# Kernel optimization log

Hardware: AMD Instinct MI355X
Metric: run time of the kernel (lower is better)

Reference implementation:

```python
import jax, jax.numpy as jnp
import numpy as np
import math

D_MODEL = 768
D_STATE = 16
D_CONV = 4
EXPAND = 2
D_INNER = EXPAND * D_MODEL
DT_RANK = math.ceil(D_MODEL / 16)
B_SZ, SEQ = 2, 2048


def setup_inputs() -> dict:
    key = jax.random.key(0)
    ks = jax.random.split(key, 10)
    s = 0.02
    inp = {
        "input_states": jax.random.normal(ks[0], (B_SZ, SEQ, D_MODEL), jnp.float32),
        "in_proj_w": jax.random.normal(ks[1], (2 * D_INNER, D_MODEL), jnp.float32) * s,
        "conv_w": jax.random.normal(ks[2], (D_INNER, 1, D_CONV), jnp.float32) * s,
        "conv_b": jnp.zeros((D_INNER,), jnp.float32),
        "x_proj_w": jax.random.normal(ks[3], (DT_RANK + 2 * D_STATE, D_INNER), jnp.float32) * s,
        "dt_proj_w": jax.random.normal(ks[4], (D_INNER, DT_RANK), jnp.float32) * s,
        "dt_proj_b": jax.random.normal(ks[5], (D_INNER,), jnp.float32) * 0.1,
        # S4D-real style init: A_log = log(1..d_state) per channel
        "A_log": jnp.log(jnp.broadcast_to(jnp.arange(1, D_STATE + 1, dtype=jnp.float32), (D_INNER, D_STATE))),
        "D": jnp.ones((D_INNER,), jnp.float32),
        "out_proj_w": jax.random.normal(ks[6], (D_MODEL, D_INNER), jnp.float32) * s,
        "context_len": 2,
    }
    return inp


def _silu(x):
    return x * jax.nn.sigmoid(x)


def _chain_tree_scan(w, x):
    # first-order linear recurrence h_t = w_t * h_{t-1} + x_t along last axis
    # (w_0 is ignored by construction of the associative combine)
    def comb(l, r):
        al, bl = l
        ar, br = r
        return (ar * al, ar * bl + br)
    _, h = jax.lax.associative_scan(comb, (w, x), axis=-1)
    return h


def reference(input_states, in_proj_w, conv_w, conv_b, x_proj_w,
              dt_proj_w, dt_proj_b, A_log, D, out_proj_w, context_len):
    # context_len == 2 -> chain-tree branch (identity BFS order, parent[i]=i-1)
    b, L, dm = input_states.shape
    di, n = A_log.shape[0], A_log.shape[1]

    proj = jnp.einsum('bld,ed->ble', input_states, in_proj_w)  # [b,l,2*di]
    proj = jnp.transpose(proj, (0, 2, 1))                      # [b,2*di,l]
    hidden, gate = jnp.split(proj, 2, axis=1)                  # each [b,di,l]

    # causal depthwise conv1d (pad left d_conv-1, truncate to seq_len)
    hidden = jax.lax.conv_general_dilated(
        hidden, conv_w, window_strides=(1,), padding=[(D_CONV - 1, 0)],
        dimension_numbers=('NCH', 'OIH', 'NCH'), feature_group_count=di)
    hidden = _silu(hidden + conv_b[None, :, None])             # [b,di,l]

    ssm = jnp.einsum('bdl,ed->ble', hidden, x_proj_w)          # [b,l,dt_rank+2n]
    dt, Bm, Cm = jnp.split(ssm, [DT_RANK, DT_RANK + n], axis=-1)
    dt = jax.nn.softplus(jnp.einsum('blr,dr->bld', dt, dt_proj_w) + dt_proj_b)
    dt = jnp.transpose(dt, (0, 2, 1))                          # [b,di,l]

    A = -jnp.exp(A_log.astype(jnp.float32))                    # [di,n]
    dA = jnp.exp(A[None, :, None, :] * dt[:, :, :, None])      # [b,di,l,n]
    dBu = dt[:, :, :, None] * Bm[:, None, :, :] * hidden[:, :, :, None]  # [b,di,l,n]

    # rearrange 'b d l n -> b (d n) l'
    w = jnp.transpose(dA, (0, 1, 3, 2)).reshape(b, di * n, L)
    fin = jnp.transpose(dBu, (0, 1, 3, 2)).reshape(b, di * n, L)

    fin_f = jnp.flip(fin, axis=-1)
    w_f = jnp.roll(jnp.flip(w, axis=-1), 1, axis=-1)

    h = _chain_tree_scan(w_f, fin_f)
    # feature_out2 (edge_weight == w_f via identity gather) * 0.3 + feature_out1
    fout = 1.3 * h

    fout = jnp.flip(fout, axis=-1)                              # [b,(d n),l]
    fout = fout.reshape(b, di, n, L)
    fout = jnp.transpose(fout, (0, 3, 1, 2))                    # [b,l,d,n]

    scan_out = jnp.einsum('bldn,bln->bld', fout, Cm)            # [b,l,di]
    scan_out = jnp.transpose(scan_out, (0, 2, 1))               # [b,di,l]

    y = scan_out + hidden * D[None, :, None]
    y = y * _silu(gate)
    out = jnp.einsum('bdl,ed->ble', y, out_proj_w)              # [b,l,d_model]
    return out
```

## Files before the change

kernel.cpp:

```cpp
#include <hip/hip_runtime.h>
#include <hip/hip_bf16.h>

#define DI     1536
#define DM     768
#define E2     3072
#define NST    16
#define LSEQ   2048
#define NB     2
#define NLB    4096
#define SSMW   80
#define DTRANK 48
#define NC     32
#define CP     64

typedef unsigned short u16;
typedef unsigned int   u32;
typedef __attribute__((ext_vector_type(8))) __bf16 bf16x8;
typedef __attribute__((ext_vector_type(4))) float  f32x4;

__device__ __forceinline__ float b2f(u16 u) {
  union { u32 i; float f; } v; v.i = ((u32)u) << 16; return v.f;
}
__device__ __forceinline__ u16 f2b(float f) {
  union { float f; u32 i; } v; v.f = f;
  u32 r = v.i + 0x7FFFu + ((v.i >> 16) & 1u);
  return (u16)(r >> 16);
}
__device__ __forceinline__ void gld16(const u16* g, u16* l) {
  __builtin_amdgcn_global_load_lds(
      (const __attribute__((address_space(1))) void*)g,
      (__attribute__((address_space(3))) void*)l, 16, 0, 0);
}
__device__ __forceinline__ float silu_f(float x) {
  return x / (1.f + __expf(-x));
}

#define B2F_LO(w) __uint_as_float(((u32)(w)) << 16)
#define B2F_HI(w) __uint_as_float(((u32)(w)) & 0xFFFF0000u)

#define ROWSUM16(p)                                                                               \
  asm("v_add_f32 %0, %1, %2 row_ror:8 row_mask:0xf bank_mask:0xf" : "=v"(p) : "v"(p), "v"(p));    \
  asm("v_add_f32 %0, %1, %2 row_ror:4 row_mask:0xf bank_mask:0xf" : "=v"(p) : "v"(p), "v"(p));    \
  asm("v_add_f32 %0, %1, %2 row_ror:2 row_mask:0xf bank_mask:0xf" : "=v"(p) : "v"(p), "v"(p));    \
  asm("v_add_f32 %0, %1, %2 row_ror:1 row_mask:0xf bank_mask:0xf" : "=v"(p) : "v"(p), "v"(p));

__global__ __launch_bounds__(256) void castk(const float* __restrict__ in,
                                             u16* __restrict__ out, int n) {
  int i = (blockIdx.x * 256 + threadIdx.x) * 4;
  if (i >= n) return;
  float4 v = *(const float4*)(in + i);
  u32 lo = (u32)f2b(v.x) | ((u32)f2b(v.y) << 16);
  u32 hi = (u32)f2b(v.z) | ((u32)f2b(v.w) << 16);
  uint2 pk; pk.x = lo; pk.y = hi;
  *(uint2*)(out + i) = pk;
}

__global__ __launch_bounds__(256) void castwdt(const float* __restrict__ in,
                                               const float* __restrict__ bias,
                                               u16* __restrict__ out) {
  int i = blockIdx.x * 256 + threadIdx.x;
  int row = i >> 6, col = i & 63;
  float v = (col < 48) ? in[row * 48 + col] : (col == 48 ? bias[row] : 0.f);
  out[i] = f2b(v);
}

template<int CMODE>
__global__ __launch_bounds__(256) void gemm_bt(const u16* __restrict__ A,
                                               const u16* __restrict__ B,
                                               void* __restrict__ Cp,
                                               int M, int N, int K) {
  __shared__ __align__(16) u16 a_s[128 * 32];
  __shared__ __align__(16) u16 b_s[128 * 32];
  const int tid = threadIdx.x, lane = tid & 63, w = tid >> 6;
  const int m0 = blockIdx.x * 128, n0 = blockIdx.y * 128;
  const int wm = w >> 1, wn = w & 1;
  f32x4 acc[4][4];
#pragma unroll
  for (int i = 0; i < 4; i++)
#pragma unroll
    for (int j = 0; j < 4; j++) acc[i][j] = (f32x4){0.f, 0.f, 0.f, 0.f};

  const int rA = lane >> 2;
  const int c8 = (lane & 3) * 8;
  const int fr = lane & 15;
  const int fk = (lane >> 4) * 8;

  for (int k0 = 0; k0 < K; k0 += 32) {
#pragma unroll
    for (int j = 0; j < 2; j++) {
      int rr = (w * 2 + j) * 16;
      gld16(A + (size_t)(m0 + rr + rA) * K + k0 + c8, a_s + rr * 32);
      gld16(B + (size_t)(n0 + rr + rA) * K + k0 + c8, b_s + rr * 32);
    }
    __syncthreads();
    bf16x8 af[4], bf[4];
#pragma unroll
    for (int mi = 0; mi < 4; mi++)
      af[mi] = *(const bf16x8*)(a_s + (wm * 64 + mi * 16 + fr) * 32 + fk);
#pragma unroll
    for (int ni = 0; ni < 4; ni++)
      bf[ni] = *(const bf16x8*)(b_s + (wn * 64 + ni * 16 + fr) * 32 + fk);
#pragma unroll
    for (int mi = 0; mi < 4; mi++)
#pragma unroll
      for (int ni = 0; ni < 4; ni++)
        acc[mi][ni] = __builtin_amdgcn_mfma_f32_16x16x32_bf16(
            af[mi], bf[ni], acc[mi][ni], 0, 0, 0);
    __syncthreads();
  }

  const int rbase = (lane >> 4) * 4, cbase = lane & 15;
#pragma unroll
  for (int mi = 0; mi < 4; mi++)
#pragma unroll
    for (int ni = 0; ni < 4; ni++)
#pragma unroll
      for (int j = 0; j < 4; j++) {
        int m = m0 + wm * 64 + mi * 16 + rbase + j;
        int n = n0 + wn * 64 + ni * 16 + cbase;
        float v = acc[mi][ni][j];
        if (CMODE == 0) {
          u16* C = (u16*)Cp;
          C[((size_t)(n >> 11) * E2 + m) * LSEQ + (n & 2047)] = f2b(v);
        } else if (CMODE == 1) {
          float* C = (float*)Cp;
          C[(size_t)m * N + n] = v;
        } else {
          float sp = (v > 20.f) ? v : log1pf(__expf(v));
          u16* C = (u16*)Cp;
          C[(size_t)n * DI + m] = f2b(sp);
        }
      }
}

__global__ __launch_bounds__(256) void gemm_xproj(const u16* __restrict__ A,
                                                  const u16* __restrict__ B,
                                                  float* __restrict__ C,
                                                  u16* __restrict__ dtin) {
  __shared__ __align__(16) u16 a_s[128 * 32];
  __shared__ __align__(16) u16 b_s[128 * 32];
  const int tid = threadIdx.x, lane = tid & 63, w = tid >> 6;
  const int n0 = blockIdx.x * 128;
  const int K = DI;
  f32x4 acc[5][2];
#pragma unroll
  for (int i = 0; i < 5; i++) { acc[i][0] = (f32x4){0,0,0,0}; acc[i][1] = (f32x4){0,0,0,0}; }

  const int rA = lane >> 2;
  const int c8 = (lane & 3) * 8;
  const int fr = lane & 15;
  const int fk = (lane >> 4) * 8;

  for (int k0 = 0; k0 < K; k0 += 32) {
#pragma unroll
    for (int j = 0; j < 2; j++) {
      int rr = (w * 2 + j) * 16;
      gld16(A + (size_t)(rr + rA) * K + k0 + c8, a_s + rr * 32);
      gld16(B + (size_t)(n0 + rr + rA) * K + k0 + c8, b_s + rr * 32);
    }
    __syncthreads();
    bf16x8 af[5], bf[2];
#pragma unroll
    for (int mi = 0; mi < 5; mi++)
      af[mi] = *(const bf16x8*)(a_s + (mi * 16 + fr) * 32 + fk);
#pragma unroll
    for (int ni = 0; ni < 2; ni++)
      bf[ni] = *(const bf16x8*)(b_s + (w * 32 + ni * 16 + fr) * 32 + fk);
#pragma unroll
    for (int mi = 0; mi < 5; mi++)
#pragma unroll
      for (int ni = 0; ni < 2; ni++)
        acc[mi][ni] = __builtin_amdgcn_mfma_f32_16x16x32_bf16(
            af[mi], bf[ni], acc[mi][ni], 0, 0, 0);
    __syncthreads();
  }

  const int rbase = (lane >> 4) * 4, cbase = lane & 15;
#pragma unroll
  for (int mi = 0; mi < 5; mi++)
#pragma unroll
    for (int ni = 0; ni < 2; ni++)
#pragma unroll
      for (int j = 0; j < 4; j++) {
        int m = mi * 16 + rbase + j;
        int n = n0 + w * 32 + ni * 16 + cbase;
        float v = acc[mi][ni][j];
        C[(size_t)n * SSMW + m] = v;
        if (m < 64) {
          u16 dv = (m < 48) ? f2b(v) : (m == 48 ? f2b(1.0f) : (u16)0);
          dtin[(size_t)n * 64 + m] = dv;
        }
      }
}

__global__ __launch_bounds__(256) void conv_silu(const u16* __restrict__ proj,
                                                 const float* __restrict__ cw,
                                                 const float* __restrict__ cb,
                                                 u16* __restrict__ hidden) {
  __shared__ __align__(16) u16 in_s[64][96];
  __shared__ __align__(16) u16 o_s[64][64];
  const int t = threadIdx.x;
  const int d0 = blockIdx.x * 64, l0 = blockIdx.y * 64, bb = blockIdx.z;

  for (int c = t; c < 64 * 12; c += 256) {
    int r = c / 12, q = c % 12;
    int gl = l0 - 32 + q * 8;
    uint4 v;
    if (gl >= 0) v = *(const uint4*)(proj + ((size_t)bb * E2 + d0 + r) * LSEQ + gl);
    else         v = (uint4){0u, 0u, 0u, 0u};
    *(uint4*)(&in_s[r][q * 8]) = v;
  }
  __syncthreads();

  const int dd = t >> 2, ls = t & 3;
  const int d = d0 + dd;
  const float w0 = cw[d * 4 + 0], w1 = cw[d * 4 + 1], w2 = cw[d * 4 + 2], w3 = cw[d * 4 + 3];
  const float bias = cb[d];
#pragma unroll
  for (int i = 0; i < 16; i++) {
    int li = ls * 16 + i;
    int base = 32 + li - 3;
    float h = w0 * b2f(in_s[dd][base + 0]) + w1 * b2f(in_s[dd][base + 1]) +
              w2 * b2f(in_s[dd][base + 2]) + w3 * b2f(in_s[dd][base + 3]) + bias;
    o_s[li][dd] = f2b(silu_f(h));
  }
  __syncthreads();

  for (int c = t; c < 512; c += 256) {
    int r = c >> 3, q = c & 7;
    *(uint4*)(hidden + ((size_t)bb * LSEQ + l0 + r) * DI + d0 + q * 8) =
        *(const uint4*)(&o_s[r][q * 8]);
  }
}

__global__ __launch_bounds__(256) void scan_sum(const u16* __restrict__ dt,
                                                const u16* __restrict__ hidden,
                                                const float* __restrict__ ssm,
                                                const float* __restrict__ A_log,
                                                float* __restrict__ gsum,
                                                float* __restrict__ sdt) {
  __shared__ __align__(16) u16 dt_t[16][80];
  __shared__ __align__(16) u16 hid_t[16][80];
  __shared__ __align__(16) float B_t[16][68];
  const int t = threadIdx.x;
  const int d0 = blockIdx.x * 16, c = blockIdx.y, bb = blockIdx.z;
  const int dl = t >> 4, n = t & 15;
  const int d = d0 + dl;
  const int l0 = c * CP;
  {
    int r = t >> 2, q = t & 3;
    size_t lbrow = (size_t)bb * LSEQ + l0 + r;
    uint2 dv = *(const uint2*)(dt + lbrow * DI + d0 + q * 4);
    uint2 hv = *(const uint2*)(hidden + lbrow * DI + d0 + q * 4);
    float4 bv = *(const float4*)(ssm + lbrow * SSMW + 48 + q * 4);
    dt_t[q * 4 + 0][r] = (u16)dv.x;  dt_t[q * 4 + 1][r] = (u16)(dv.x >> 16);
    dt_t[q * 4 + 2][r] = (u16)dv.y;  dt_t[q * 4 + 3][r] = (u16)(dv.y >> 16);
    hid_t[q * 4 + 0][r] = (u16)hv.x; hid_t[q * 4 + 1][r] = (u16)(hv.x >> 16);
    hid_t[q * 4 + 2][r] = (u16)hv.y; hid_t[q * 4 + 3][r] = (u16)(hv.y >> 16);
    B_t[q * 4 + 0][r] = bv.x; B_t[q * 4 + 1][r] = bv.y;
    B_t[q * 4 + 2][r] = bv.z; B_t[q * 4 + 3][r] = bv.w;
  }
  const float An = -__expf(A_log[d * 16 + n]);
  float dt_prev = (c == NC - 1) ? 0.f
                : b2f(dt[((size_t)bb * LSEQ + l0 + CP) * DI + d]);
  __syncthreads();
  float g = 0.f, sumdt = 0.f;
#define STEPS(dtv_, hv_, Bv_) {            \
    float dtv = dtv_;                      \
    float dA = __expf(An * dt_prev);       \
    g = dtv * (Bv_) * (hv_) + dA * g;      \
    sumdt += dt_prev;                      \
    dt_prev = dtv; }
#pragma unroll
  for (int s = 7; s >= 0; --s) {
    uint4 d8 = *(const uint4*)(&dt_t[dl][s * 8]);
    uint4 h8 = *(const uint4*)(&hid_t[dl][s * 8]);
    f32x4 b0 = *(const f32x4*)(&B_t[n][s * 8]);
    f32x4 b1 = *(const f32x4*)(&B_t[n][s * 8 + 4]);
    STEPS(B2F_HI(d8.w), B2F_HI(h8.w), b1[3]);
    STEPS(B2F_LO(d8.w), B2F_LO(h8.w), b1[2]);
    STEPS(B2F_HI(d8.z), B2F_HI(h8.z), b1[1]);
    STEPS(B2F_LO(d8.z), B2F_LO(h8.z), b1[0]);
    STEPS(B2F_HI(d8.y), B2F_HI(h8.y), b0[3]);
    STEPS(B2F_LO(d8.y), B2F_LO(h8.y), b0[2]);
    STEPS(B2F_HI(d8.x), B2F_HI(h8.x), b0[1]);
    STEPS(B2F_LO(d8.x), B2F_LO(h8.x), b0[0]);
  }
#undef STEPS
  size_t idx = (((size_t)bb * NC + c) * DI + d) * 16 + n;
  gsum[idx] = g;
  sdt[idx]  = sumdt;
}

__global__ __launch_bounds__(256) void scan_carry(const float* __restrict__ gsum,
                                                  const float* __restrict__ sdt,
                                                  const float* __restrict__ A_log,
                                                  float* __restrict__ carry) {
  const int t = blockIdx.x * 256 + threadIdx.x;
  const int bb = blockIdx.y;
  const int d = t >> 4, n = t & 15;
  const float An = -__expf(A_log[d * 16 + n]);
  float cg = 0.f;
  carry[(((size_t)bb * NC + NC - 1) * DI + d) * 16 + n] = 0.f;
  for (int c = NC - 2; c >= 0; --c) {
    size_t up = (((size_t)bb * NC + (c + 1)) * DI + d) * 16 + n;
    cg = gsum[up] + __expf(An * sdt[up]) * cg;
    carry[(((size_t)bb * NC + c) * DI + d) * 16 + n] = cg;
  }
}

__global__ __launch_bounds__(256) void scan_apply(const u16* __restrict__ proj,
                                                  const u16* __restrict__ hidden,
                                                  const u16* __restrict__ dt,
                                                  const float* __restrict__ ssm,
                                                  const float* __restrict__ A_log,
                                                  const float* __restrict__ Dp,
                                                  const float* __restrict__ carry,
                                                  u16* __restrict__ y) {
  __shared__ __align__(16) u16 dt_t[16][80];
  __shared__ __align__(16) u16 hid_t[16][80];
  __shared__ __align__(16) u16 gate_t[16][80];
  __shared__ __align__(16) float B_t[16][68];
  __shared__ __align__(16) float C_t[16][68];
  __shared__ __align__(16) u16 y_s[64][16];
  const int t = threadIdx.x;
  const int d0 = blockIdx.x * 16, c = blockIdx.y, bb = blockIdx.z;
  const int dl = t >> 4, n = t & 15;
  const int d = d0 + dl;
  const int l0 = c * CP;
  {
    int r = t >> 2, q = t & 3;
    size_t lbrow = (size_t)bb * LSEQ + l0 + r;
    uint2 dv = *(const uint2*)(dt + lbrow * DI + d0 + q * 4);
    uint2 hv = *(const uint2*)(hidden + lbrow * DI + d0 + q * 4);
    float4 bv = *(const float4*)(ssm + lbrow * SSMW + 48 + q * 4);
    float4 cv = *(const float4*)(ssm + lbrow * SSMW + 64 + q * 4);
    dt_t[q * 4 + 0][r] = (u16)dv.x;  dt_t[q * 4 + 1][r] = (u16)(dv.x >> 16);
    dt_t[q * 4 + 2][r] = (u16)dv.y;  dt_t[q * 4 + 3][r] = (u16)(dv.y >> 16);
    hid_t[q * 4 + 0][r] = (u16)hv.x; hid_t[q * 4 + 1][r] = (u16)(hv.x >> 16);
    hid_t[q * 4 + 2][r] = (u16)hv.y; hid_t[q * 4 + 3][r] = (u16)(hv.y >> 16);
    B_t[q * 4 + 0][r] = bv.x; B_t[q * 4 + 1][r] = bv.y;
    B_t[q * 4 + 2][r] = bv.z; B_t[q * 4 + 3][r] = bv.w;
    C_t[q * 4 + 0][r] = cv.x; C_t[q * 4 + 1][r] = cv.y;
    C_t[q * 4 + 2][r] = cv.z; C_t[q * 4 + 3][r] = cv.w;
  }
  {
    int r = t >> 4, q = t & 15;
    *(uint2*)(&gate_t[r][q * 4]) =
        *(const uint2*)(proj + ((size_t)bb * E2 + DI + d0 + r) * LSEQ + l0 + q * 4);
  }
  const float An = -__expf(A_log[d * 16 + n]);
  const float Dd = Dp[d];
  float g = carry[(((size_t)bb * NC + c) * DI + d) * 16 + n];
  float dt_prev = (c == NC - 1) ? 0.f
                : b2f(dt[((size_t)bb * LSEQ + l0 + CP) * DI + d]);
  __syncthreads();
  float pcap[4] = {0.f, 0.f, 0.f, 0.f};
  float hcap[4] = {0.f, 0.f, 0.f, 0.f};
#define STEPA(IDX, dtv_, hv_, Bv_, Cv_) {                  \
    float dtv = dtv_; float hvv = hv_;                     \
    float dA = __expf(An * dt_prev);                       \
    g = dtv * (Bv_) * hvv + dA * g;                        \
    float p = g * (Cv_);                                   \
    ROWSUM16(p);                                           \
    if (n == ((IDX) & 15)) {                               \
      pcap[(IDX) >> 4] = p; hcap[(IDX) >> 4] = hvv;        \
    }                                                      \
    dt_prev = dtv; }
#pragma unroll
  for (int s = 7; s >= 0; --s) {
    uint4 d8 = *(const uint4*)(&dt_t[dl][s * 8]);
    uint4 h8 = *(const uint4*)(&hid_t[dl][s * 8]);
    f32x4 b0 = *(const f32x4*)(&B_t[n][s * 8]);
    f32x4 b1 = *(const f32x4*)(&B_t[n][s * 8 + 4]);
    f32x4 c0 = *(const f32x4*)(&C_t[n][s * 8]);
    f32x4 c1 = *(const f32x4*)(&C_t[n][s * 8 + 4]);
    STEPA(s * 8 + 7, B2F_HI(d8.w), B2F_HI(h8.w), b1[3], c1[3]);
    STEPA(s * 8 + 6, B2F_LO(d8.w), B2F_LO(h8.w), b1[2], c1[2]);
    STEPA(s * 8 + 5, B2F_HI(d8.z), B2F_HI(h8.z), b1[1], c1[1]);
    STEPA(s * 8 + 4, B2F_LO(d8.z), B2F_LO(h8.z), b1[0], c1[0]);
    STEPA(s * 8 + 3, B2F_HI(d8.y), B2F_HI(h8.y), b0[3], c0[3]);
    STEPA(s * 8 + 2, B2F_LO(d8.y), B2F_LO(h8.y), b0[2], c0[2]);
    STEPA(s * 8 + 1, B2F_HI(d8.x), B2F_HI(h8.x), b0[1], c0[1]);
    STEPA(s * 8 + 0, B2F_LO(d8.x), B2F_LO(h8.x), b0[0], c0[0]);
  }
#undef STEPA
#pragma unroll
  for (int j2 = 0; j2 < 4; ++j2) {
    float gv = b2f(gate_t[dl][n + 16 * j2]);
    float yv = (1.3f * pcap[j2] + hcap[j2] * Dd) * silu_f(gv);
    y_s[n + 16 * j2][dl] = f2b(yv);
  }
  __syncthreads();
  {
    int r = t >> 2, q = t & 3;
    *(uint2*)(y + ((size_t)bb * LSEQ + l0 + r) * DI + d0 + q * 4) =
        *(const uint2*)(&y_s[r][q * 4]);
  }
}

extern "C" void kernel_launch(void* const* d_in, const int* in_sizes, int n_in,
                              void* d_out, int out_size, void* d_ws, size_t ws_size,
                              hipStream_t stream) {
  const float* x_in   = (const float*)d_in[0];
  const float* w_in   = (const float*)d_in[1];
  const float* conv_w = (const float*)d_in[2];
  const float* conv_b = (const float*)d_in[3];
  const float* w_x    = (const float*)d_in[4];
  const float* w_dt   = (const float*)d_in[5];
  const float* b_dt   = (const float*)d_in[6];
  const float* A_log  = (const float*)d_in[7];
  const float* Dp     = (const float*)d_in[8];
  const float* w_out  = (const float*)d_in[9];
  float* outp = (float*)d_out;

  size_t off = 0;
  auto carve = [&](size_t bytes) {
    void* p = (char*)d_ws + off;
    off += (bytes + 255) & ~(size_t)255;
    return p;
  };
  u16*   in_b   = (u16*)  carve((size_t)NLB * DM * 2);
  u16*   win_b  = (u16*)  carve((size_t)E2 * DM * 2);
  u16*   wout_b = (u16*)  carve((size_t)DM * DI * 2);
  u16*   wx_b   = (u16*)  carve((size_t)SSMW * DI * 2);
  u16*   wdtp_b = (u16*)  carve((size_t)DI * 64 * 2);
  u16*   proj_b = (u16*)  carve((size_t)NB * E2 * LSEQ * 2);
  u16*   hid_b  = (u16*)  carve((size_t)NLB * DI * 2);
  float* ssm_b  = (float*)carve((size_t)NLB * SSMW * 4);
  u16*   dtin_b = (u16*)  carve((size_t)NLB * 64 * 2);
  u16*   dt_b   = (u16*)  carve((size_t)NLB * DI * 2);
  u16*   y_b    = (u16*)  carve((size_t)NLB * DI * 2);
  float* gsum_b = (float*)carve((size_t)NB * NC * DI * 16 * 4);
  float* sdt_b  = (float*)carve((size_t)NB * NC * DI * 16 * 4);
  float* car_b  = (float*)carve((size_t)NB * NC * DI * 16 * 4);

  castk<<<NLB * DM / 1024, 256, 0, stream>>>(x_in, in_b, NLB * DM);
  castk<<<E2 * DM / 1024, 256, 0, stream>>>(w_in, win_b, E2 * DM);
  castk<<<DM * DI / 1024, 256, 0, stream>>>(w_out, wout_b, DM * DI);
  castk<<<SSMW * DI / 1024, 256, 0, stream>>>(w_x, wx_b, SSMW * DI);
  castwdt<<<DI * 64 / 256, 256, 0, stream>>>(w_dt, b_dt, wdtp_b);

  gemm_bt<0><<<dim3(E2 / 128, NLB / 128), 256, 0, stream>>>(
      win_b, in_b, proj_b, E2, NLB, DM);
  conv_silu<<<dim3(DI / 64, LSEQ / 64, NB), 256, 0, stream>>>(
      proj_b, conv_w, conv_b, hid_b);
  gemm_xproj<<<NLB / 128, 256, 0, stream>>>(wx_b, hid_b, ssm_b, dtin_b);

  gemm_bt<2><<<dim3(DI / 128, NLB / 128), 256, 0, stream>>>(
      wdtp_b, dtin_b, dt_b, DI, NLB, 64);

  scan_sum<<<dim3(DI / 16, NC, NB), 256, 0, stream>>>(
      dt_b, hid_b, ssm_b, A_log, gsum_b, sdt_b);
  scan_carry<<<dim3(DI * 16 / 256, NB), 256, 0, stream>>>(
      gsum_b, sdt_b, A_log, car_b);
  scan_apply<<<dim3(DI / 16, NC, NB), 256, 0, stream>>>(
      proj_b, hid_b, dt_b, ssm_b, A_log, Dp, car_b, y_b);

  gemm_bt<1><<<dim3(NLB / 128, DM / 128), 256, 0, stream>>>(
      y_b, wout_b, outp, NLB, DM, DI);
}
```

Baseline: 336.7 us.

## Fuse cast kernels, stage dt GEMM output through LDS, use exp2 in scan

Merges the four fp32-to-bf16 cast launches into one kernel that dispatches on a flat index range, removing launch overhead. The dt-projection GEMM epilogue now writes softplus results into a shared-memory tile and stores them as coalesced 16-byte rows, replacing scattered 2-byte strided stores. The scan kernels fold log2(e) into the A coefficient and call exp2f instead of __expf. This costs extra LDS and barriers in the dt epilogue.

```diff
diff --git a/kernel.cpp b/kernel.cpp
--- a/kernel.cpp
+++ b/kernel.cpp
@@ -12,6 +12,7 @@
 #define DTRANK 48
 #define NC     32
 #define CP     64
+#define LOG2E  1.44269504f
 
 typedef unsigned short u16;
 typedef unsigned int   u32;
@@ -44,15 +45,27 @@
   asm("v_add_f32 %0, %1, %2 row_ror:2 row_mask:0xf bank_mask:0xf" : "=v"(p) : "v"(p), "v"(p));    \
   asm("v_add_f32 %0, %1, %2 row_ror:1 row_mask:0xf bank_mask:0xf" : "=v"(p) : "v"(p), "v"(p));
 
-__global__ __launch_bounds__(256) void castk(const float* __restrict__ in,
-                                             u16* __restrict__ out, int n) {
+__global__ __launch_bounds__(256) void castall(const float* __restrict__ x_in,
+                                               const float* __restrict__ w_in,
+                                               const float* __restrict__ w_out,
+                                               const float* __restrict__ w_x,
+                                               u16* __restrict__ in_b,
+                                               u16* __restrict__ win_b,
+                                               u16* __restrict__ wout_b,
+                                               u16* __restrict__ wx_b) {
   int i = (blockIdx.x * 256 + threadIdx.x) * 4;
-  if (i >= n) return;
-  float4 v = *(const float4*)(in + i);
+  const int n1 = NLB * DM, n2 = n1 + E2 * DM, n3 = n2 + DM * DI, n4 = n3 + SSMW * DI;
+  const float* src; u16* dst; int off;
+  if (i < n1)      { src = x_in;  dst = in_b;   off = i; }
+  else if (i < n2) { src = w_in;  dst = win_b;  off = i - n1; }
+  else if (i < n3) { src = w_out; dst = wout_b; off = i - n2; }
+  else if (i < n4) { src = w_x;   dst = wx_b;   off = i - n3; }
+  else return;
+  float4 v = *(const float4*)(src + off);
   u32 lo = (u32)f2b(v.x) | ((u32)f2b(v.y) << 16);
   u32 hi = (u32)f2b(v.z) | ((u32)f2b(v.w) << 16);
   uint2 pk; pk.x = lo; pk.y = hi;
-  *(uint2*)(out + i) = pk;
+  *(uint2*)(dst + off) = pk;
 }
 
 __global__ __launch_bounds__(256) void castwdt(const float* __restrict__ in,
@@ -71,6 +84,7 @@
                                                int M, int N, int K) {
   __shared__ __align__(16) u16 a_s[128 * 32];
   __shared__ __align__(16) u16 b_s[128 * 32];
+  __shared__ __align__(16) u16 t_s[(CMODE == 2) ? 64 * 128 : 1];
   const int tid = threadIdx.x, lane = tid & 63, w = tid >> 6;
   const int m0 = blockIdx.x * 128, n0 = blockIdx.y * 128;
   const int wm = w >> 1, wn = w & 1;
@@ -110,6 +124,34 @@
   }
 
   const int rbase = (lane >> 4) * 4, cbase = lane & 15;
+  if (CMODE == 2) {
+    u16* dt = (u16*)Cp;
+#pragma unroll
+    for (int pass = 0; pass < 2; ++pass) {
+      if (wn == pass) {
+#pragma unroll
+        for (int mi = 0; mi < 4; mi++)
+#pragma unroll
+          for (int ni = 0; ni < 4; ni++)
+#pragma unroll
+            for (int j = 0; j < 4; j++) {
+              int ml = wm * 64 + mi * 16 + rbase + j;
+              int nl = ni * 16 + cbase;
+              float v = acc[mi][ni][j];
+              float sp = (v > 20.f) ? v : log1pf(__expf(v));
+              t_s[nl * 128 + ml] = f2b(sp);
+            }
+      }
+      __syncthreads();
+      for (int c = tid; c < 64 * 16; c += 256) {
+        int nl = c >> 4, q = c & 15;
+        int n = n0 + pass * 64 + nl;
+        *(uint4*)(dt + (size_t)n * DI + m0 + q * 8) = *(const uint4*)(&t_s[nl * 128 + q * 8]);
+      }
+      __syncthreads();
+    }
+    return;
+  }
 #pragma unroll
   for (int mi = 0; mi < 4; mi++)
 #pragma unroll
@@ -122,13 +164,9 @@
         if (CMODE == 0) {
           u16* C = (u16*)Cp;
           C[((size_t)(n >> 11) * E2 + m) * LSEQ + (n & 2047)] = f2b(v);
-        } else if (CMODE == 1) {
+        } else {
           float* C = (float*)Cp;
           C[(size_t)m * N + n] = v;
-        } else {
-          float sp = (v > 20.f) ? v : log1pf(__expf(v));
-          u16* C = (u16*)Cp;
-          C[(size_t)n * DI + m] = f2b(sp);
         }
       }
 }
@@ -260,14 +298,14 @@
     B_t[q * 4 + 0][r] = bv.x; B_t[q * 4 + 1][r] = bv.y;
     B_t[q * 4 + 2][r] = bv.z; B_t[q * 4 + 3][r] = bv.w;
   }
-  const float An = -__expf(A_log[d * 16 + n]);
+  const float An2 = -__expf(A_log[d * 16 + n]) * LOG2E;
   float dt_prev = (c == NC - 1) ? 0.f
                 : b2f(dt[((size_t)bb * LSEQ + l0 + CP) * DI + d]);
   __syncthreads();
   float g = 0.f, sumdt = 0.f;
 #define STEPS(dtv_, hv_, Bv_) {            \
     float dtv = dtv_;                      \
-    float dA = __expf(An * dt_prev);       \
+    float dA = exp2f(An2 * dt_prev);       \
     g = dtv * (Bv_) * (hv_) + dA * g;      \
     sumdt += dt_prev;                      \
     dt_prev = dtv; }
@@ -299,12 +337,12 @@
   const int t = blockIdx.x * 256 + threadIdx.x;
   const int bb = blockIdx.y;
   const int d = t >> 4, n = t & 15;
-  const float An = -__expf(A_log[d * 16 + n]);
+  const float An2 = -__expf(A_log[d * 16 + n]) * LOG2E;
   float cg = 0.f;
   carry[(((size_t)bb * NC + NC - 1) * DI + d) * 16 + n] = 0.f;
   for (int c = NC - 2; c >= 0; --c) {
     size_t up = (((size_t)bb * NC + (c + 1)) * DI + d) * 16 + n;
-    cg = gsum[up] + __expf(An * sdt[up]) * cg;
+    cg = gsum[up] + exp2f(An2 * sdt[up]) * cg;
     carry[(((size_t)bb * NC + c) * DI + d) * 16 + n] = cg;
   }
 }
@@ -349,7 +387,7 @@
     *(uint2*)(&gate_t[r][q * 4]) =
         *(const uint2*)(proj + ((size_t)bb * E2 + DI + d0 + r) * LSEQ + l0 + q * 4);
   }
-  const float An = -__expf(A_log[d * 16 + n]);
+  const float An2 = -__expf(A_log[d * 16 + n]) * LOG2E;
   const float Dd = Dp[d];
   float g = carry[(((size_t)bb * NC + c) * DI + d) * 16 + n];
   float dt_prev = (c == NC - 1) ? 0.f
@@ -359,7 +397,7 @@
   float hcap[4] = {0.f, 0.f, 0.f, 0.f};
 #define STEPA(IDX, dtv_, hv_, Bv_, Cv_) {                  \
     float dtv = dtv_; float hvv = hv_;                     \
-    float dA = __expf(An * dt_prev);                       \
+    float dA = exp2f(An2 * dt_prev);                       \
     g = dtv * (Bv_) * hvv + dA * g;                        \
     float p = g * (Cv_);                                   \
     ROWSUM16(p);                                           \
@@ -435,10 +473,8 @@
   float* sdt_b  = (float*)carve((size_t)NB * NC * DI * 16 * 4);
   float* car_b  = (float*)carve((size_t)NB * NC * DI * 16 * 4);
 
-  castk<<<NLB * DM / 1024, 256, 0, stream>>>(x_in, in_b, NLB * DM);
-  castk<<<E2 * DM / 1024, 256, 0, stream>>>(w_in, win_b, E2 * DM);
-  castk<<<DM * DI / 1024, 256, 0, stream>>>(w_out, wout_b, DM * DI);
-  castk<<<SSMW * DI / 1024, 256, 0, stream>>>(w_x, wx_b, SSMW * DI);
+  castall<<<(NLB * DM + E2 * DM + DM * DI + SSMW * DI) / 1024, 256, 0, stream>>>(
+      x_in, w_in, w_out, w_x, in_b, win_b, wout_b, wx_b);
   castwdt<<<DI * 64 / 256, 256, 0, stream>>>(w_dt, b_dt, wdtp_b);
 
   gemm_bt<0><<<dim3(E2 / 128, NLB / 128), 256, 0, stream>>>(
```

Result: no change. 342.8 us (+1.8%).
